# Optimization experiments

Measured on AMD Instinct MI355X. Metric: run time of the kernel, lower is better.

The kernel has to match this reference:

```python
import jax, jax.numpy as jnp
import numpy as np

N_NODES = 50000
DIM = 128
N_EDGES = 800000
N_UID = 4096
ORDER = 3
LN_EPS = 1e-5


def setup_inputs() -> dict:
    key = jax.random.key(0)
    ks = jax.random.split(key, 6)
    scale = 1.0 / np.sqrt(DIM)
    embedding = jax.random.normal(ks[0], (N_NODES, DIM), jnp.float32) * np.sqrt(2.0 / DIM)  # kaiming-ish
    W = jax.random.normal(ks[1], (ORDER, DIM, DIM), jnp.float32) * scale
    b = jnp.zeros((ORDER, DIM), jnp.float32)
    gamma = jnp.ones((ORDER, DIM), jnp.float32)
    beta = jnp.zeros((ORDER, DIM), jnp.float32)
    src = jax.random.randint(ks[2], (N_EDGES,), 0, N_NODES, jnp.int32)
    dst = jax.random.randint(ks[3], (N_EDGES,), 0, N_NODES, jnp.int32)
    uid = jax.random.randint(ks[4], (N_UID,), 0, N_NODES, jnp.int32)
    return {"embedding": embedding, "W": W, "b": b, "gamma": gamma,
            "beta": beta, "src": src, "dst": dst, "uid": uid}


def _layer_norm(x, g, bta):
    mu = jnp.mean(x, axis=-1, keepdims=True)
    var = jnp.var(x, axis=-1, keepdims=True)
    return (x - mu) * jax.lax.rsqrt(var + LN_EPS) * g + bta


def reference(embedding, W, b, gamma, beta, src, dst, uid):
    # in-degree per destination node (DGL 'gcn' aggregator uses in_degrees)
    deg = jax.ops.segment_sum(jnp.ones((src.shape[0],), embedding.dtype), dst,
                              num_segments=N_NODES)  # [N]
    inv = (1.0 / (deg + 1.0))[:, None]  # [N,1]
    feats = embedding
    for i in range(ORDER):
        # gather source features, scatter-sum into destinations
        neigh = jax.ops.segment_sum(feats[src], dst, num_segments=N_NODES)  # [N,D]
        h = (neigh + feats) * inv                    # gcn-style mean incl. self
        h = jnp.einsum('nd,ed->ne', h, W[i]) + b[i]  # fc_neigh
        feats = jax.nn.elu(_layer_norm(h, gamma[i], beta[i]))
    return feats[uid]  # [N_UID, D]
```

## Files before the change

kernel.cpp:

```cpp
#include <hip/hip_runtime.h>
#include <math.h>

typedef unsigned int   uint;
typedef unsigned short ushort;

#define N_NODES 50000
#define DIM     128
#define N_EDGES 800000
#define N_UID   4096
#define LN_EPS  1e-5f
#define RST     132
#define XST     136
#define NBUCK   196
#define PCHUNK  4096

typedef __attribute__((ext_vector_type(8))) short bf16x8;
typedef __attribute__((ext_vector_type(4))) float f32x4;
typedef __attribute__((ext_vector_type(4))) uint  u32x4;

__device__ __forceinline__ float bf_lo(uint u) { return __builtin_bit_cast(float, u << 16); }
__device__ __forceinline__ float bf_hi(uint u) { return __builtin_bit_cast(float, u & 0xffff0000u); }
__device__ __forceinline__ uint pack_bf16(float a, float b) {
    uint ua = __builtin_bit_cast(uint, a);
    uint ub = __builtin_bit_cast(uint, b);
    uint ra = (ua + 0x7fffu + ((ua >> 16) & 1u)) >> 16;
    uint rb = (ub + 0x7fffu + ((ub >> 16) & 1u)) >> 16;
    return ra | (rb << 16);
}

__global__ __launch_bounds__(256) void prep_kernel(const float* __restrict__ emb, ushort* __restrict__ E,
                                                   const float* __restrict__ W, ushort* __restrict__ WB,
                                                   int* __restrict__ bhist) {
    int i = blockIdx.x * 256 + threadIdx.x;
    if (i < N_NODES * DIM / 4) {
        const float4 v = ((const float4*)emb)[i];
        uint2 p;
        p.x = pack_bf16(v.x, v.y);
        p.y = pack_bf16(v.z, v.w);
        ((uint2*)E)[i] = p;
    }
    if (i < 3 * DIM * DIM / 4) {
        const float4 v = ((const float4*)W)[i];
        uint2 p;
        p.x = pack_bf16(v.x, v.y);
        p.y = pack_bf16(v.z, v.w);
        ((uint2*)WB)[i] = p;
    }
    if (i < NBUCK) bhist[i] = 0;
}

__global__ __launch_bounds__(256) void bhist_kernel(const int* __restrict__ dst, int* __restrict__ bhist) {
    __shared__ int h[256];
    const int t = threadIdx.x;
    h[t] = 0;
    __syncthreads();
    for (int e = blockIdx.x * 256 + t; e < N_EDGES; e += gridDim.x * 256)
        atomicAdd(&h[dst[e] >> 8], 1);
    __syncthreads();
    if (t < NBUCK && h[t]) atomicAdd(&bhist[t], h[t]);
}

__global__ __launch_bounds__(256) void bscan_kernel(const int* __restrict__ bhist, int* __restrict__ bbase,
                                                    int* __restrict__ bcur, int* __restrict__ off) {
    __shared__ int sh[256];
    const int t = threadIdx.x;
    const int v = (t < NBUCK) ? bhist[t] : 0;
    sh[t] = v;
    __syncthreads();
    for (int o = 1; o < 256; o <<= 1) {
        int x = (t >= o) ? sh[t - o] : 0;
        __syncthreads();
        sh[t] += x;
        __syncthreads();
    }
    const int excl = sh[t] - v;
    if (t < NBUCK) { bbase[t] = excl; bcur[t] = excl; }
    if (t == NBUCK - 1) bbase[NBUCK] = excl + v;
    if (t == 0) off[N_NODES] = N_EDGES;
}

__global__ __launch_bounds__(256) void part_kernel(const int* __restrict__ src, const int* __restrict__ dst,
                                                   int* __restrict__ bcur, int2* __restrict__ pak) {
    __shared__ int h[256];
    __shared__ int base[256];
    __shared__ int cur[256];
    const int t  = threadIdx.x;
    const int e0 = blockIdx.x * PCHUNK;
    const int e1 = min(e0 + PCHUNK, N_EDGES);
    h[t] = 0;
    __syncthreads();
    for (int i = e0 + t; i < e1; i += 256)
        atomicAdd(&h[dst[i] >> 8], 1);
    __syncthreads();
    if (t < NBUCK && h[t]) base[t] = atomicAdd(&bcur[t], h[t]);
    cur[t] = 0;
    __syncthreads();
    for (int i = e0 + t; i < e1; i += 256) {
        const int s = src[i], d = dst[i];
        const int b = d >> 8;
        const int q = atomicAdd(&cur[b], 1);
        pak[base[b] + q] = make_int2(s, d);
    }
}

__global__ __launch_bounds__(256) void bucket_kernel(const int2* __restrict__ pak, const int* __restrict__ bbase,
                                                     int* __restrict__ off, int* __restrict__ csr) {
    __shared__ int cnt[256];
    __shared__ int pos[256];
    const int b = blockIdx.x, t = threadIdx.x;
    const int e0 = bbase[b], e1 = bbase[b + 1], m = e1 - e0;
    cnt[t] = 0;
    __syncthreads();
    for (int i = t; i < m; i += 256) atomicAdd(&cnt[pak[e0 + i].y & 255], 1);
    __syncthreads();
    const int v = cnt[t];
    pos[t] = v;
    __syncthreads();
    for (int o = 1; o < 256; o <<= 1) {
        int x = (t >= o) ? pos[t - o] : 0;
        __syncthreads();
        pos[t] += x;
        __syncthreads();
    }
    const int excl = pos[t] - v;
    const int node = b * 256 + t;
    if (node < N_NODES) off[node] = e0 + excl;
    __syncthreads();
    pos[t] = excl;
    __syncthreads();
    for (int i = t; i < m; i += 256) {
        const int2 p = pak[e0 + i];
        const int q = atomicAdd(&pos[p.y & 255], 1);
        csr[e0 + q] = p.x;
    }
}

template <bool OUT_BF16>
__global__ __launch_bounds__(512) void layer_kernel(
    const ushort* __restrict__ fin, void* __restrict__ fout,
    const int* __restrict__ off, const int* __restrict__ csr,
    const int* __restrict__ uidmap, const ushort* __restrict__ wb,
    const float* __restrict__ bias, const float* __restrict__ gamma,
    const float* __restrict__ beta, int nrows)
{
    __shared__ ushort xs[32 * XST];
    __shared__ float  ys[32 * RST];
    const int t = threadIdx.x;
    const int rows = blockIdx.x * 32;

    {
        const int lx   = t & 15;
        const int st   = t >> 4;
        const int slot = rows + st;
        const bool valid = slot < nrows;
        const int n  = valid ? (uidmap ? uidmap[slot] : slot) : 0;
        const int d0 = off[n];
        int d1 = off[n + 1];
        if (!valid) d1 = d0;
        const int deg = d1 - d0;

        float a[8];
        {
            const uint4 q = ((const uint4*)(fin + (size_t)n * DIM))[lx];
            a[0]=bf_lo(q.x); a[1]=bf_hi(q.x); a[2]=bf_lo(q.y); a[3]=bf_hi(q.y);
            a[4]=bf_lo(q.z); a[5]=bf_hi(q.z); a[6]=bf_lo(q.w); a[7]=bf_hi(q.w);
        }

        const int nfull = deg >> 3;
        int e = d0;
        int id[8];
        if (nfull > 0) {
            #pragma unroll
            for (int k = 0; k < 8; ++k) id[k] = csr[e + k];
        }
        for (int r = 0; r < nfull; ++r) {
            uint4 v[8];
            #pragma unroll
            for (int k = 0; k < 8; ++k)
                v[k] = ((const uint4*)(fin + (size_t)id[k] * DIM))[lx];
            int idn[8];
            if (r + 1 < nfull) {
                #pragma unroll
                for (int k = 0; k < 8; ++k) idn[k] = csr[e + 8 + k];
            }
            #pragma unroll
            for (int k = 0; k < 8; ++k) {
                a[0] += bf_lo(v[k].x); a[1] += bf_hi(v[k].x);
                a[2] += bf_lo(v[k].y); a[3] += bf_hi(v[k].y);
                a[4] += bf_lo(v[k].z); a[5] += bf_hi(v[k].z);
                a[6] += bf_lo(v[k].w); a[7] += bf_hi(v[k].w);
            }
            if (r + 1 < nfull) {
                #pragma unroll
                for (int k = 0; k < 8; ++k) id[k] = idn[k];
            }
            e += 8;
        }
        if (e < d1) {
            const int last = d1 - 1;
            int   idt[8];
            float m[8];
            #pragma unroll
            for (int k = 0; k < 8; ++k) {
                const int ee = e + k;
                idt[k] = csr[(ee <= last) ? ee : last];
                m[k]   = (ee <= last) ? 1.0f : 0.0f;
            }
            uint4 v[8];
            #pragma unroll
            for (int k = 0; k < 8; ++k)
                v[k] = ((const uint4*)(fin + (size_t)idt[k] * DIM))[lx];
            #pragma unroll
            for (int k = 0; k < 8; ++k) {
                a[0] = fmaf(m[k], bf_lo(v[k].x), a[0]); a[1] = fmaf(m[k], bf_hi(v[k].x), a[1]);
                a[2] = fmaf(m[k], bf_lo(v[k].y), a[2]); a[3] = fmaf(m[k], bf_hi(v[k].y), a[3]);
                a[4] = fmaf(m[k], bf_lo(v[k].z), a[4]); a[5] = fmaf(m[k], bf_hi(v[k].z), a[5]);
                a[6] = fmaf(m[k], bf_lo(v[k].w), a[6]); a[7] = fmaf(m[k], bf_hi(v[k].w), a[7]);
            }
        }

        const float iv = 1.0f / (float)(deg + 1);
        uint4 p;
        p.x = pack_bf16(a[0] * iv, a[1] * iv);
        p.y = pack_bf16(a[2] * iv, a[3] * iv);
        p.z = pack_bf16(a[4] * iv, a[5] * iv);
        p.w = pack_bf16(a[6] * iv, a[7] * iv);
        *((uint4*)(xs + st * XST + lx * 8)) = p;
    }
    __syncthreads();

    {
        const int wave = t >> 6, lane = t & 63;
        const int row_off = (wave >> 2) * 16;
        const int col_off = (wave & 3) * 32;
        const int lm   = lane & 15;
        const int quad = lane >> 4;
        f32x4 acc[2] = {f32x4{0,0,0,0}, f32x4{0,0,0,0}};
        const ushort* xrow = xs + (row_off + lm) * XST + quad * 8;
        const ushort* __restrict__ wrow = wb + (size_t)(col_off + lm) * DIM + quad * 8;
        #pragma unroll
        for (int kk = 0; kk < 4; ++kk) {
            const bf16x8 af = __builtin_bit_cast(bf16x8, *(const u32x4*)(xrow + kk * 32));
            #pragma unroll
            for (int c = 0; c < 2; ++c) {
                const bf16x8 bf = __builtin_bit_cast(bf16x8,
                    *(const u32x4*)(wrow + (size_t)c * 16 * DIM + kk * 32));
                acc[c] = __builtin_amdgcn_mfma_f32_16x16x32_bf16(af, bf, acc[c], 0, 0, 0);
            }
        }
        #pragma unroll
        for (int c = 0; c < 2; ++c) {
            #pragma unroll
            for (int r = 0; r < 4; ++r)
                ys[(row_off + quad * 4 + r) * RST + col_off + c * 16 + lm] = acc[c][r];
        }
    }
    __syncthreads();

    {
        const int r   = t >> 4;
        const int seg = t & 15;
        const int db  = seg * 8;
        const float* yr = ys + r * RST + db;
        float vs[8];
        {
            const float4 y0 = ((const float4*)yr)[0];
            const float4 y1 = ((const float4*)yr)[1];
            const float4 b0 = ((const float4*)(bias + db))[0];
            const float4 b1 = ((const float4*)(bias + db))[1];
            vs[0] = y0.x + b0.x; vs[1] = y0.y + b0.y; vs[2] = y0.z + b0.z; vs[3] = y0.w + b0.w;
            vs[4] = y1.x + b1.x; vs[5] = y1.y + b1.y; vs[6] = y1.z + b1.z; vs[7] = y1.w + b1.w;
        }
        float s1 = 0.0f, s2 = 0.0f;
        #pragma unroll
        for (int i = 0; i < 8; ++i) { s1 += vs[i]; s2 += vs[i] * vs[i]; }
        #pragma unroll
        for (int m = 1; m < 16; m <<= 1) {
            s1 += __shfl_xor(s1, m);
            s2 += __shfl_xor(s2, m);
        }
        const float mu  = s1 * (1.0f / 128.0f);
        const float var = s2 * (1.0f / 128.0f) - mu * mu;
        const float rs  = rsqrtf(var + LN_EPS);
        float ov[8];
        {
            const float4 g0 = ((const float4*)(gamma + db))[0];
            const float4 g1 = ((const float4*)(gamma + db))[1];
            const float4 t0 = ((const float4*)(beta + db))[0];
            const float4 t1 = ((const float4*)(beta + db))[1];
            float z;
            z = (vs[0] - mu) * rs * g0.x + t0.x; ov[0] = (z > 0.0f) ? z : expm1f(z);
            z = (vs[1] - mu) * rs * g0.y + t0.y; ov[1] = (z > 0.0f) ? z : expm1f(z);
            z = (vs[2] - mu) * rs * g0.z + t0.z; ov[2] = (z > 0.0f) ? z : expm1f(z);
            z = (vs[3] - mu) * rs * g0.w + t0.w; ov[3] = (z > 0.0f) ? z : expm1f(z);
            z = (vs[4] - mu) * rs * g1.x + t1.x; ov[4] = (z > 0.0f) ? z : expm1f(z);
            z = (vs[5] - mu) * rs * g1.y + t1.y; ov[5] = (z > 0.0f) ? z : expm1f(z);
            z = (vs[6] - mu) * rs * g1.z + t1.z; ov[6] = (z > 0.0f) ? z : expm1f(z);
            z = (vs[7] - mu) * rs * g1.w + t1.w; ov[7] = (z > 0.0f) ? z : expm1f(z);
        }
        const int n = rows + r;
        if (n < nrows) {
            if (OUT_BF16) {
                uint4 p;
                p.x = pack_bf16(ov[0], ov[1]);
                p.y = pack_bf16(ov[2], ov[3]);
                p.z = pack_bf16(ov[4], ov[5]);
                p.w = pack_bf16(ov[6], ov[7]);
                *((uint4*)((ushort*)fout + (size_t)n * DIM + db)) = p;
            } else {
                float* op = (float*)fout + (size_t)n * DIM + db;
                ((float4*)op)[0] = make_float4(ov[0], ov[1], ov[2], ov[3]);
                ((float4*)op)[1] = make_float4(ov[4], ov[5], ov[6], ov[7]);
            }
        }
    }
}

extern "C" void kernel_launch(void* const* d_in, const int* in_sizes, int n_in,
                              void* d_out, int out_size, void* d_ws, size_t ws_size,
                              hipStream_t stream) {
    const float* emb   = (const float*)d_in[0];
    const float* W     = (const float*)d_in[1];
    const float* bias  = (const float*)d_in[2];
    const float* gamma = (const float*)d_in[3];
    const float* beta  = (const float*)d_in[4];
    const int*   src   = (const int*)d_in[5];
    const int*   dst   = (const int*)d_in[6];
    const int*   uid   = (const int*)d_in[7];

    ushort* E    = (ushort*)d_ws;
    ushort* A    = E + (size_t)N_NODES * DIM;
    ushort* B    = A + (size_t)N_NODES * DIM;
    ushort* WB   = B + (size_t)N_NODES * DIM;
    int*    off  = (int*)(WB + 3 * DIM * DIM);
    int*    bhist = off + (N_NODES + 4);
    int*    bbase = bhist + 256;
    int*    bcur  = bbase + 260;
    int2*   pak   = (int2*)(bcur + 256);
    int*    csr   = (int*)(pak + N_EDGES);

    prep_kernel<<<(N_NODES * DIM / 4 + 255) / 256, 256, 0, stream>>>(emb, E, W, WB, bhist);
    bhist_kernel<<<512, 256, 0, stream>>>(dst, bhist);
    bscan_kernel<<<1, 256, 0, stream>>>(bhist, bbase, bcur, off);
    part_kernel<<<(N_EDGES + PCHUNK - 1) / PCHUNK, 256, 0, stream>>>(src, dst, bcur, pak);
    bucket_kernel<<<NBUCK, 256, 0, stream>>>(pak, bbase, off, csr);

    const int lblk = (N_NODES + 31) / 32;
    layer_kernel<true><<<lblk, 512, 0, stream>>>(E, A, off, csr, nullptr, WB,
                                                 bias, gamma, beta, N_NODES);
    layer_kernel<true><<<lblk, 512, 0, stream>>>(A, B, off, csr, nullptr, WB + DIM * DIM,
                                                 bias + DIM, gamma + DIM, beta + DIM, N_NODES);
    layer_kernel<false><<<N_UID / 32, 512, 0, stream>>>(B, (float*)d_out, off, csr, uid,
                                                        WB + 2 * DIM * DIM, bias + 2 * DIM,
                                                        gamma + 2 * DIM, beta + 2 * DIM, N_UID);
}
```

Baseline: 230.5 us.

## Sort nodes by degree for layer load balance and fuse preprocessing kernels

Builds a degree histogram in the bucket kernel and a new counting-sort kernel that produces a degree-sorted node permutation. The first two layer kernels then process nodes in that order, so rows with similar degrees share a block and wavefronts waste less time on divergent neighbour loops. Output is scattered back to original node positions. Separately, the conversion and histogram kernels are merged, and the single-block scan is folded redundantly into the partition and bucket kernels, which removes launches. The cost is an extra kernel, a memset, and scattered output writes.

Result: no change. 233.7 us (+1.4%).

```diff
diff --git a/kernel.cpp b/kernel.cpp
--- a/kernel.cpp
+++ b/kernel.cpp
@@ -13,6 +13,7 @@
 #define XST     136
 #define NBUCK   196
 #define PCHUNK  4096
+#define DBINS   128
 
 typedef __attribute__((ext_vector_type(8))) short bf16x8;
 typedef __attribute__((ext_vector_type(4))) float f32x4;
@@ -28,72 +29,62 @@
     return ra | (rb << 16);
 }
 
-__global__ __launch_bounds__(256) void prep_kernel(const float* __restrict__ emb, ushort* __restrict__ E,
-                                                   const float* __restrict__ W, ushort* __restrict__ WB,
-                                                   int* __restrict__ bhist) {
-    int i = blockIdx.x * 256 + threadIdx.x;
-    if (i < N_NODES * DIM / 4) {
+__global__ __launch_bounds__(256) void cvthist_kernel(const float* __restrict__ emb, ushort* __restrict__ E,
+                                                      const float* __restrict__ W, ushort* __restrict__ WB,
+                                                      const int* __restrict__ dst, int* __restrict__ bhist) {
+    __shared__ int h[256];
+    const int t = threadIdx.x;
+    h[t] = 0;
+    __syncthreads();
+    const int gsz = gridDim.x * 256;
+    for (int i = blockIdx.x * 256 + t; i < N_NODES * DIM / 4; i += gsz) {
         const float4 v = ((const float4*)emb)[i];
         uint2 p;
         p.x = pack_bf16(v.x, v.y);
         p.y = pack_bf16(v.z, v.w);
         ((uint2*)E)[i] = p;
     }
-    if (i < 3 * DIM * DIM / 4) {
-        const float4 v = ((const float4*)W)[i];
-        uint2 p;
-        p.x = pack_bf16(v.x, v.y);
-        p.y = pack_bf16(v.z, v.w);
-        ((uint2*)WB)[i] = p;
-    }
-    if (i < NBUCK) bhist[i] = 0;
-}
-
-__global__ __launch_bounds__(256) void bhist_kernel(const int* __restrict__ dst, int* __restrict__ bhist) {
-    __shared__ int h[256];
-    const int t = threadIdx.x;
-    h[t] = 0;
-    __syncthreads();
-    for (int e = blockIdx.x * 256 + t; e < N_EDGES; e += gridDim.x * 256)
+    {
+        const int i = blockIdx.x * 256 + t;
+        if (i < 3 * DIM * DIM / 4) {
+            const float4 v = ((const float4*)W)[i];
+            uint2 p;
+            p.x = pack_bf16(v.x, v.y);
+            p.y = pack_bf16(v.z, v.w);
+            ((uint2*)WB)[i] = p;
+        }
+    }
+    for (int e = blockIdx.x * 256 + t; e < N_EDGES; e += gsz)
         atomicAdd(&h[dst[e] >> 8], 1);
     __syncthreads();
     if (t < NBUCK && h[t]) atomicAdd(&bhist[t], h[t]);
 }
 
-__global__ __launch_bounds__(256) void bscan_kernel(const int* __restrict__ bhist, int* __restrict__ bbase,
-                                                    int* __restrict__ bcur, int* __restrict__ off) {
-    __shared__ int sh[256];
-    const int t = threadIdx.x;
-    const int v = (t < NBUCK) ? bhist[t] : 0;
-    sh[t] = v;
-    __syncthreads();
-    for (int o = 1; o < 256; o <<= 1) {
-        int x = (t >= o) ? sh[t - o] : 0;
-        __syncthreads();
-        sh[t] += x;
-        __syncthreads();
-    }
-    const int excl = sh[t] - v;
-    if (t < NBUCK) { bbase[t] = excl; bcur[t] = excl; }
-    if (t == NBUCK - 1) bbase[NBUCK] = excl + v;
-    if (t == 0) off[N_NODES] = N_EDGES;
-}
-
 __global__ __launch_bounds__(256) void part_kernel(const int* __restrict__ src, const int* __restrict__ dst,
-                                                   int* __restrict__ bcur, int2* __restrict__ pak) {
+                                                   const int* __restrict__ bhist, int* __restrict__ bcur,
+                                                   int2* __restrict__ pak) {
+    __shared__ int sc[256];
     __shared__ int h[256];
     __shared__ int base[256];
     __shared__ int cur[256];
-    const int t  = threadIdx.x;
+    const int t = threadIdx.x;
+    const int v = (t < NBUCK) ? bhist[t] : 0;
+    sc[t] = v;
+    h[t] = 0; cur[t] = 0;
+    __syncthreads();
+    for (int o = 1; o < 256; o <<= 1) {
+        int x = (t >= o) ? sc[t - o] : 0;
+        __syncthreads();
+        sc[t] += x;
+        __syncthreads();
+    }
+    const int excl = sc[t] - v;
     const int e0 = blockIdx.x * PCHUNK;
     const int e1 = min(e0 + PCHUNK, N_EDGES);
-    h[t] = 0;
-    __syncthreads();
     for (int i = e0 + t; i < e1; i += 256)
         atomicAdd(&h[dst[i] >> 8], 1);
     __syncthreads();
-    if (t < NBUCK && h[t]) base[t] = atomicAdd(&bcur[t], h[t]);
-    cur[t] = 0;
+    if (t < NBUCK && h[t]) base[t] = excl + atomicAdd(&bcur[t], h[t]);
     __syncthreads();
     for (int i = e0 + t; i < e1; i += 256) {
         const int s = src[i], d = dst[i];
@@ -103,18 +94,32 @@
     }
 }
 
-__global__ __launch_bounds__(256) void bucket_kernel(const int2* __restrict__ pak, const int* __restrict__ bbase,
-                                                     int* __restrict__ off, int* __restrict__ csr) {
+__global__ __launch_bounds__(256) void bucket_kernel(const int2* __restrict__ pak, const int* __restrict__ bhist,
+                                                     int* __restrict__ off, int* __restrict__ csr,
+                                                     int* __restrict__ dhist) {
+    __shared__ int sc[256];
     __shared__ int cnt[256];
     __shared__ int pos[256];
+    __shared__ int dh[DBINS];
     const int b = blockIdx.x, t = threadIdx.x;
-    const int e0 = bbase[b], e1 = bbase[b + 1], m = e1 - e0;
+    const int bv = (t < NBUCK) ? bhist[t] : 0;
+    sc[t] = bv;
     cnt[t] = 0;
-    __syncthreads();
+    if (t < DBINS) dh[t] = 0;
+    __syncthreads();
+    for (int o = 1; o < 256; o <<= 1) {
+        int x = (t >= o) ? sc[t - o] : 0;
+        __syncthreads();
+        sc[t] += x;
+        __syncthreads();
+    }
+    const int e0 = (b == 0) ? 0 : sc[b - 1];
+    const int e1 = sc[b];
+    const int m = e1 - e0;
     for (int i = t; i < m; i += 256) atomicAdd(&cnt[pak[e0 + i].y & 255], 1);
     __syncthreads();
-    const int v = cnt[t];
-    pos[t] = v;
+    const int c = cnt[t];
+    pos[t] = c;
     __syncthreads();
     for (int o = 1; o < 256; o <<= 1) {
         int x = (t >= o) ? pos[t - o] : 0;
@@ -122,10 +127,15 @@
         pos[t] += x;
         __syncthreads();
     }
-    const int excl = pos[t] - v;
+    const int excl = pos[t] - c;
     const int node = b * 256 + t;
-    if (node < N_NODES) off[node] = e0 + excl;
-    __syncthreads();
+    if (node < N_NODES) {
+        off[node] = e0 + excl;
+        atomicAdd(&dh[min(c, DBINS - 1)], 1);
+    }
+    if (b == 0 && t == 0) off[N_NODES] = N_EDGES;
+    __syncthreads();
+    if (t < DBINS && dh[t]) atomicAdd(&dhist[t], dh[t]);
     pos[t] = excl;
     __syncthreads();
     for (int i = t; i < m; i += 256) {
@@ -135,16 +145,54 @@
     }
 }
 
-template <bool OUT_BF16>
+__global__ __launch_bounds__(256) void dscat_kernel(const int* __restrict__ off, const int* __restrict__ dhist,
+                                                    int* __restrict__ dcur, int* __restrict__ perm) {
+    __shared__ int sc[DBINS];
+    __shared__ int dv[DBINS];
+    __shared__ int lh[DBINS];
+    __shared__ int lbase[DBINS];
+    __shared__ int lcur[DBINS];
+    const int b = blockIdx.x, t = threadIdx.x;
+    if (t < DBINS) { lh[t] = 0; lcur[t] = 0; }
+    __syncthreads();
+    const int node = b * 256 + t;
+    int bin = -1;
+    if (node < N_NODES) {
+        const int deg = off[node + 1] - off[node];
+        bin = min(deg, DBINS - 1);
+        atomicAdd(&lh[bin], 1);
+    }
+    __syncthreads();
+    if (t < DBINS) { dv[t] = dhist[t]; sc[t] = dv[t]; }
+    __syncthreads();
+    for (int o = 1; o < DBINS; o <<= 1) {
+        int x = (t >= o && t < DBINS) ? sc[t - o] : 0;
+        __syncthreads();
+        if (t < DBINS) sc[t] += x;
+        __syncthreads();
+    }
+    if (t < DBINS) {
+        const int excl = sc[t] - dv[t];
+        if (lh[t]) lbase[t] = excl + atomicAdd(&dcur[t], lh[t]);
+    }
+    __syncthreads();
+    if (node < N_NODES) {
+        const int q = atomicAdd(&lcur[bin], 1);
+        perm[lbase[bin] + q] = node;
+    }
+}
+
+template <bool OUT_BF16, bool PERMOUT>
 __global__ __launch_bounds__(512) void layer_kernel(
     const ushort* __restrict__ fin, void* __restrict__ fout,
     const int* __restrict__ off, const int* __restrict__ csr,
-    const int* __restrict__ uidmap, const ushort* __restrict__ wb,
+    const int* __restrict__ nodemap, const ushort* __restrict__ wb,
     const float* __restrict__ bias, const float* __restrict__ gamma,
     const float* __restrict__ beta, int nrows)
 {
     __shared__ ushort xs[32 * XST];
     __shared__ float  ys[32 * RST];
+    __shared__ int    nid[32];
     const int t = threadIdx.x;
     const int rows = blockIdx.x * 32;
 
@@ -153,7 +201,8 @@
         const int st   = t >> 4;
         const int slot = rows + st;
         const bool valid = slot < nrows;
-        const int n  = valid ? (uidmap ? uidmap[slot] : slot) : 0;
+        const int n  = valid ? (nodemap ? nodemap[slot] : slot) : 0;
+        if (lx == 0) nid[st] = n;
         const int d0 = off[n];
         int d1 = off[n + 1];
         if (!valid) d1 = d0;
@@ -298,17 +347,18 @@
             z = (vs[6] - mu) * rs * g1.z + t1.z; ov[6] = (z > 0.0f) ? z : expm1f(z);
             z = (vs[7] - mu) * rs * g1.w + t1.w; ov[7] = (z > 0.0f) ? z : expm1f(z);
         }
-        const int n = rows + r;
-        if (n < nrows) {
+        const int slot3 = rows + r;
+        if (slot3 < nrows) {
+            const int nout = PERMOUT ? nid[r] : slot3;
             if (OUT_BF16) {
                 uint4 p;
                 p.x = pack_bf16(ov[0], ov[1]);
                 p.y = pack_bf16(ov[2], ov[3]);
                 p.z = pack_bf16(ov[4], ov[5]);
                 p.w = pack_bf16(ov[6], ov[7]);
-                *((uint4*)((ushort*)fout + (size_t)n * DIM + db)) = p;
+                *((uint4*)((ushort*)fout + (size_t)nout * DIM + db)) = p;
             } else {
-                float* op = (float*)fout + (size_t)n * DIM + db;
+                float* op = (float*)fout + (size_t)nout * DIM + db;
                 ((float4*)op)[0] = make_float4(ov[0], ov[1], ov[2], ov[3]);
                 ((float4*)op)[1] = make_float4(ov[4], ov[5], ov[6], ov[7]);
             }
@@ -328,29 +378,32 @@
     const int*   dst   = (const int*)d_in[6];
     const int*   uid   = (const int*)d_in[7];
 
-    ushort* E    = (ushort*)d_ws;
-    ushort* A    = E + (size_t)N_NODES * DIM;
-    ushort* B    = A + (size_t)N_NODES * DIM;
-    ushort* WB   = B + (size_t)N_NODES * DIM;
-    int*    off  = (int*)(WB + 3 * DIM * DIM);
-    int*    bhist = off + (N_NODES + 4);
-    int*    bbase = bhist + 256;
-    int*    bcur  = bbase + 260;
-    int2*   pak   = (int2*)(bcur + 256);
+    ushort* E     = (ushort*)d_ws;
+    ushort* A     = E + (size_t)N_NODES * DIM;
+    ushort* B     = A + (size_t)N_NODES * DIM;
+    ushort* WB    = B + (size_t)N_NODES * DIM;
+    int*    off   = (int*)(WB + 3 * DIM * DIM);
+    int*    aux   = off + (N_NODES + 4);
+    int*    bhist = aux;
+    int*    bcur  = aux + 256;
+    int*    dhist = aux + 512;
+    int*    dcur  = aux + 640;
+    int*    perm  = aux + 768;
+    int2*   pak   = (int2*)(perm + N_NODES);
     int*    csr   = (int*)(pak + N_EDGES);
 
-    prep_kernel<<<(N_NODES * DIM / 4 + 255) / 256, 256, 0, stream>>>(emb, E, W, WB, bhist);
-    bhist_kernel<<<512, 256, 0, stream>>>(dst, bhist);
-    bscan_kernel<<<1, 256, 0, stream>>>(bhist, bbase, bcur, off);
-    part_kernel<<<(N_EDGES + PCHUNK - 1) / PCHUNK, 256, 0, stream>>>(src, dst, bcur, pak);
-    bucket_kernel<<<NBUCK, 256, 0, stream>>>(pak, bbase, off, csr);
+    hipMemsetAsync(aux, 0, 768 * sizeof(int), stream);
+    cvthist_kernel<<<512, 256, 0, stream>>>(emb, E, W, WB, dst, bhist);
+    part_kernel<<<(N_EDGES + PCHUNK - 1) / PCHUNK, 256, 0, stream>>>(src, dst, bhist, bcur, pak);
+    bucket_kernel<<<NBUCK, 256, 0, stream>>>(pak, bhist, off, csr, dhist);
+    dscat_kernel<<<NBUCK, 256, 0, stream>>>(off, dhist, dcur, perm);
 
     const int lblk = (N_NODES + 31) / 32;
-    layer_kernel<true><<<lblk, 512, 0, stream>>>(E, A, off, csr, nullptr, WB,
-                                                 bias, gamma, beta, N_NODES);
-    layer_kernel<true><<<lblk, 512, 0, stream>>>(A, B, off, csr, nullptr, WB + DIM * DIM,
-                                                 bias + DIM, gamma + DIM, beta + DIM, N_NODES);
-    layer_kernel<false><<<N_UID / 32, 512, 0, stream>>>(B, (float*)d_out, off, csr, uid,
-                                                        WB + 2 * DIM * DIM, bias + 2 * DIM,
-                                                        gamma + 2 * DIM, beta + 2 * DIM, N_UID);
-}
+    layer_kernel<true, true><<<lblk, 512, 0, stream>>>(E, A, off, csr, perm, WB,
+                                                       bias, gamma, beta, N_NODES);
+    layer_kernel<true, true><<<lblk, 512, 0, stream>>>(A, B, off, csr, perm, WB + DIM * DIM,
+                                                       bias + DIM, gamma + DIM, beta + DIM, N_NODES);
+    layer_kernel<false, false><<<N_UID / 32, 512, 0, stream>>>(B, (float*)d_out, off, csr, uid,
+                                                               WB + 2 * DIM * DIM, bias + 2 * DIM,
+                                                               gamma + 2 * DIM, beta + 2 * DIM, N_UID);
+}
```
